# Kernel tuning notes

Hardware: AMD Instinct MI355X
Metric: run time of the kernel (lower is better)

## Reference

```python
import jax, jax.numpy as jnp
import numpy as np

T, IN, K, V = 4096, 512, 64, 64
H = K * V  # hidden_size = key_size * value_size
LN_EPS = 1e-5

def phi(x):
    return 1.0 + jax.nn.elu(x)

def mish(x):
    return x * jnp.tanh(jax.nn.softplus(x))

def setup_inputs() -> dict:
    key = jax.random.key(0)
    ks = jax.random.split(key, 12)
    def lin(k, out, inn):
        return (jax.random.normal(k, (out, inn), jnp.float32) / np.sqrt(inn).astype(np.float32))
    return {
        "x": jax.random.normal(ks[0], (T, IN), jnp.float32),
        "s0": jnp.zeros((1, K, V), jnp.float32),
        "z0": jnp.zeros((1, 1, K), jnp.float32),
        "start": jax.random.bernoulli(ks[1], 0.01, (T,)),
        "next_done": jax.random.bernoulli(ks[2], 0.01, (T,)),
        "Wk": lin(ks[3], K, IN), "Wq": lin(ks[4], K, IN),
        "Wv": lin(ks[5], V, IN), "bv": jnp.zeros((V,), jnp.float32),
        "Wskip": lin(ks[6], H, IN), "bskip": jnp.zeros((H,), jnp.float32),
        "W1": lin(ks[7], H, V), "b1": jnp.zeros((H,), jnp.float32),
        "W2": lin(ks[8], H, H), "b2": jnp.zeros((H,), jnp.float32),
        "W3": lin(ks[9], H, H), "b3": jnp.zeros((H,), jnp.float32),
        "ln_g": jnp.ones((H,), jnp.float32), "ln_b": jnp.zeros((H,), jnp.float32),
    }

def _combine(a, b):
    # associative update: later element's `start` resets accumulated (s, z)
    s1, z1, st1, d1 = a
    s2, z2, st2, d2 = b
    keep = jnp.logical_not(st2)
    return (s1 * keep + s2, z1 * keep + z2, jnp.logical_or(st2, st1), d2)

def reference(x, s0, z0, start, next_done, Wk, Wq, Wv, bv, Wskip, bskip,
              W1, b1, W2, b2, W3, b3, ln_g, ln_b):
    Tn = x.shape[0]
    k = phi(x @ Wk.T)           # [T, K]
    q = phi(x @ Wq.T)           # [T, K]
    v = x @ Wv.T + bv           # [T, V]
    kv = jnp.einsum('ti,tj->tij', k, v)  # [T, K, V]
    st = jnp.concatenate([jnp.zeros((1, 1, 1), bool), start.reshape(Tn, 1, 1)], 0)
    nd = jnp.concatenate([jnp.zeros((1, 1, 1), bool), next_done.reshape(Tn, 1, 1)], 0)
    kv = jnp.concatenate([s0, kv], 0)                        # [T+1, K, V]
    kk = jnp.concatenate([z0, k.reshape(Tn, 1, K)], 0)       # [T+1, 1, K]
    s, z, _, _ = jax.lax.associative_scan(_combine, (kv, kk, st, nd))
    s, z = s[1:], z[1:]
    numer = jnp.einsum('tij,ti->tj', s, q)                   # [T, V]
    # faithful to source: 'tzi,tj->tz' => sum_i z * sum_j q
    denom = jnp.einsum('tzi,tj->tz', z, q).clip(1e-6)        # [T, 1]
    out = numer / denom                                      # [T, V]
    h = mish(out @ W1.T + b1)
    h = mish(h @ W2.T + b2)
    h = h @ W3.T + b3
    h = h + (x @ Wskip.T + bskip)                            # mlp(out) + skip(x)
    mu = h.mean(-1, keepdims=True)
    var = ((h - mu) ** 2).mean(-1, keepdims=True)
    hn = (h - mu) / jnp.sqrt(var + LN_EPS) * ln_g + ln_b     # [T, H]
    return (hn, s, z)
```

## Files before the change

### kernel.cpp

```cpp
#include <hip/hip_runtime.h>
#include <math.h>

#define T_DIM 4096
#define IN_DIM 512
#define K_DIM 64
#define V_DIM 64
#define H_DIM 4096
#define CHUNKS 256
#define CLEN 16

typedef __attribute__((ext_vector_type(8))) short short8;
typedef __attribute__((ext_vector_type(4))) float f32x4;

__device__ __forceinline__ float phi_act(float v){
    return v > 0.f ? (v + 1.f) : (expm1f(v) + 1.f);
}
__device__ __forceinline__ float mish_act(float v){
    float sp = fmaxf(v, 0.f) + log1pf(expf(-fabsf(v)));
    return v * tanhf(sp);
}
__device__ __forceinline__ unsigned short f2bf(float f){
    union { float f; unsigned int u; } x; x.f = f;
    unsigned int u = x.u + 0x7fffu + ((x.u >> 16) & 1u);
    return (unsigned short)(u >> 16);
}

__device__ __forceinline__ void async16(const unsigned short* g, unsigned short* l){
    __builtin_amdgcn_global_load_lds(
        (const __attribute__((address_space(1))) unsigned int*)g,
        (__attribute__((address_space(3))) unsigned int*)l,
        16, 0, 0);
}

__device__ __forceinline__ short8 dsr128o(unsigned addr, int off){
    short8 d;
    asm volatile("ds_read_b128 %0, %1 offset:%2" : "=v"(d) : "v"(addr), "i"(off));
    return d;
}

#define LGKM(n)  asm volatile("s_waitcnt lgkmcnt(" #n ")" ::: "memory")
#define VMCNT(n) asm volatile("s_waitcnt vmcnt(" #n ")" ::: "memory")
#define SB0()    __builtin_amdgcn_sched_barrier(0)

#define CVT_X4   524288
#define CVT_WS   524288
#define CVT_W1   65536
#define CVT_W2   4194304
#define CVT_TOT  9502720
__global__ __launch_bounds__(256) void prep_kernel(
    const float* __restrict__ x,
    const float* __restrict__ Wk, const float* __restrict__ Wq, const float* __restrict__ Wv,
    const float* __restrict__ bv,
    float* __restrict__ kbuf, float* __restrict__ qbuf, float* __restrict__ vbuf,
    const float* __restrict__ Wskip, const float* __restrict__ W1,
    const float* __restrict__ W2, const float* __restrict__ W3,
    unsigned short* __restrict__ xb, unsigned short* __restrict__ Wskipb,
    unsigned short* __restrict__ W1b, unsigned short* __restrict__ W2b,
    unsigned short* __restrict__ W3b)
{
    __shared__ float As[16][68];
    __shared__ float Bs[16][68];
    const int bid = blockIdx.x;
    const int tid = threadIdx.x;

    if (bid < 192){
        const int which = bid >> 6;
        const float* B0 = which == 0 ? Wk : which == 1 ? Wq : Wv;
        float* Y        = which == 0 ? kbuf : which == 1 ? qbuf : vbuf;
        const int actp  = which < 2;
        const int bm    = (bid & 63) * 64;
        const int lrow  = tid >> 2;
        const int lk4   = (tid & 3) * 4;
        const int tm    = (tid >> 4) * 4;
        const int tn    = (tid & 15) * 4;
        float acc[4][4] = {};
        const float* aptr = x  + (size_t)(bm + lrow) * IN_DIM + lk4;
        const float* bptr = B0 + (size_t)lrow * IN_DIM + lk4;
        for (int k0 = 0; k0 < IN_DIM; k0 += 16){
            const float4 av  = *(const float4*)(aptr + k0);
            const float4 bv4 = *(const float4*)(bptr + k0);
            __syncthreads();
            As[lk4+0][lrow]=av.x;  As[lk4+1][lrow]=av.y;  As[lk4+2][lrow]=av.z;  As[lk4+3][lrow]=av.w;
            Bs[lk4+0][lrow]=bv4.x; Bs[lk4+1][lrow]=bv4.y; Bs[lk4+2][lrow]=bv4.z; Bs[lk4+3][lrow]=bv4.w;
            __syncthreads();
            #pragma unroll
            for (int kk = 0; kk < 16; ++kk){
                const float4 a = *(const float4*)&As[kk][tm];
                const float4 b = *(const float4*)&Bs[kk][tn];
                acc[0][0] += a.x*b.x; acc[0][1] += a.x*b.y; acc[0][2] += a.x*b.z; acc[0][3] += a.x*b.w;
                acc[1][0] += a.y*b.x; acc[1][1] += a.y*b.y; acc[1][2] += a.y*b.z; acc[1][3] += a.y*b.w;
                acc[2][0] += a.z*b.x; acc[2][1] += a.z*b.y; acc[2][2] += a.z*b.z; acc[2][3] += a.z*b.w;
                acc[3][0] += a.w*b.x; acc[3][1] += a.w*b.y; acc[3][2] += a.w*b.z; acc[3][3] += a.w*b.w;
            }
        }
        float badd[4] = {0.f, 0.f, 0.f, 0.f};
        if (which == 2){
            badd[0] = bv[tn+0]; badd[1] = bv[tn+1]; badd[2] = bv[tn+2]; badd[3] = bv[tn+3];
        }
        #pragma unroll
        for (int i = 0; i < 4; ++i){
            float r0 = acc[i][0] + badd[0];
            float r1 = acc[i][1] + badd[1];
            float r2 = acc[i][2] + badd[2];
            float r3 = acc[i][3] + badd[3];
            if (actp){ r0 = phi_act(r0); r1 = phi_act(r1); r2 = phi_act(r2); r3 = phi_act(r3); }
            *(float4*)&Y[(size_t)(bm + tm + i) * 64 + tn] = make_float4(r0, r1, r2, r3);
        }
        return;
    }

    const int nb = gridDim.x - 192;
    for (int i = (bid - 192) * 256 + tid; i < CVT_TOT; i += nb * 256){
        const float* src; unsigned short* dst; int off;
        if      (i < CVT_X4)                          { src = x;     dst = xb;     off = i; }
        else if (i < CVT_X4 + CVT_WS)                 { src = Wskip; dst = Wskipb; off = i - CVT_X4; }
        else if (i < CVT_X4 + CVT_WS + CVT_W1)        { src = W1;    dst = W1b;    off = i - CVT_X4 - CVT_WS; }
        else if (i < CVT_X4 + CVT_WS + CVT_W1 + CVT_W2){ src = W2;   dst = W2b;    off = i - CVT_X4 - CVT_WS - CVT_W1; }
        else                                          { src = W3;    dst = W3b;    off = i - CVT_X4 - CVT_WS - CVT_W1 - CVT_W2; }
        float4 v = ((const float4*)src)[off];
        ushort4 o;
        o.x = f2bf(v.x); o.y = f2bf(v.y); o.z = f2bf(v.z); o.w = f2bf(v.w);
        ((ushort4*)dst)[off] = o;
    }
}

__global__ __launch_bounds__(512, 2) void gemm256p(
    const unsigned short* __restrict__ A0, const unsigned short* __restrict__ B0, int K0,
    const unsigned short* __restrict__ A1, const unsigned short* __restrict__ B1, int K1,
    const float* __restrict__ bias0, const float* __restrict__ bias1,
    void* __restrict__ Y, int N, int act, int out_bf16)
{
    __shared__ unsigned short As[2][16384];
    __shared__ unsigned short Bs[2][16384];
    const int tid  = threadIdx.x;
    const int lane = tid & 63;
    const int w    = tid >> 6;
    const int wr   = w >> 2;
    const int wc   = w & 3;
    const int l15  = lane & 15;
    const int quad = lane >> 4;

    int bx = blockIdx.x, by = blockIdx.y;
    if (gridDim.x == 16 && gridDim.y == 16){
        const int id  = by * 16 + bx;
        const int xcd = id & 7;
        const int loc = id >> 3;
        bx = (xcd & 3) * 4 + (loc & 3);
        by = (xcd >> 2) * 8 + (loc >> 2);
    }
    const int bm = bx * 256;
    const int bn = by * 256;

    const int r0 = tid >> 3;
    const int kc = (tid & 7) ^ (r0 & 7);

    const unsigned asB = (unsigned)(size_t)&As[0][0];
    const unsigned bsB = (unsigned)(size_t)&Bs[0][0];
    const unsigned bA0 = asB + (unsigned)(((wr * 128 + l15) * 8 + ((0 + quad) ^ (l15 & 7))) * 16);
    const unsigned bA1 = asB + (unsigned)(((wr * 128 + l15) * 8 + ((4 + quad) ^ (l15 & 7))) * 16);
    const unsigned bB0 = bsB + (unsigned)(((wc * 64  + l15) * 8 + ((0 + quad) ^ (l15 & 7))) * 16);
    const unsigned bB1 = bsB + (unsigned)(((wc * 64  + l15) * 8 + ((4 + quad) ^ (l15 & 7))) * 16);

    f32x4 acc[8][4] = {};

    for (int seg = 0; seg < 2; ++seg){
        const unsigned short* A = seg ? A1 : A0;
        const unsigned short* B = seg ? B1 : B0;
        const int Kd = seg ? K1 : K0;
        if (Kd <= 0 || A == nullptr) continue;
        const int NT = Kd / 64;
        const size_t gstride = (size_t)64 * Kd;
        const unsigned short* pA = A + (size_t)bm * Kd + (size_t)r0 * Kd + kc * 8;
        const unsigned short* pB = B + (size_t)bn * Kd + (size_t)r0 * Kd + kc * 8;

        #pragma unroll
        for (int g = 0; g < 4; ++g) async16(pA + g * gstride, &As[0][(g * 512 + tid) * 8]);
        #pragma unroll
        for (int g = 0; g < 4; ++g) async16(pB + g * gstride, &Bs[0][(g * 512 + tid) * 8]);
        VMCNT(0);
        __builtin_amdgcn_s_barrier();

        for (int t = 0; t < NT; ++t){
            const unsigned bo = (unsigned)(t & 1) * 32768u;
            const unsigned aA0 = bA0 + bo, aA1 = bA1 + bo, aB0 = bB0 + bo, aB1 = bB1 + bo;
            short8 fa0[4], fa1[4], fb0[4], fb1[4];

            #pragma unroll
            for (int ni = 0; ni < 4; ++ni) fb0[ni] = dsr128o(aB0, ni * 2048);
            #pragma unroll
            for (int mi = 0; mi < 4; ++mi) fa0[mi] = dsr128o(aA0, mi * 2048);
            if (t + 1 < NT){
                const int bi = (t + 1) & 1;
                const int kn = (t + 1) * 64;
                #pragma unroll
                for (int g = 0; g < 4; ++g) async16(pA + g * gstride + kn, &As[bi][(g * 512 + tid) * 8]);
                #pragma unroll
                for (int g = 0; g < 4; ++g) async16(pB + g * gstride + kn, &Bs[bi][(g * 512 + tid) * 8]);
            }
            #pragma unroll
            for (int mi = 0; mi < 4; ++mi) fa1[mi] = dsr128o(aA0, (4 + mi) * 2048);

            __builtin_amdgcn_s_setprio(1);
            LGKM(7); SB0();
            #pragma unroll
            for (int ni = 0; ni < 4; ++ni)
                acc[0][ni] = __builtin_amdgcn_mfma_f32_16x16x32_bf16(fa0[0], fb0[ni], acc[0][ni], 0, 0, 0);
            LGKM(6); SB0();
            #pragma unroll
            for (int ni = 0; ni < 4; ++ni)
                acc[1][ni] = __builtin_amdgcn_mfma_f32_16x16x32_bf16(fa0[1], fb0[ni], acc[1][ni], 0, 0, 0);
            LGKM(5); SB0();
            #pragma unroll
            for (int ni = 0; ni < 4; ++ni)
                acc[2][ni] = __builtin_amdgcn_mfma_f32_16x16x32_bf16(fa0[2], fb0[ni], acc[2][ni], 0, 0, 0);
            LGKM(4); SB0();
            #pragma unroll
            for (int ni = 0; ni < 4; ++ni)
                acc[3][ni] = __builtin_amdgcn_mfma_f32_16x16x32_bf16(fa0[3], fb0[ni], acc[3][ni], 0, 0, 0);
            __builtin_amdgcn_s_setprio(0);

            #pragma unroll
            for (int ni = 0; ni < 4; ++ni) fb1[ni] = dsr128o(aB1, ni * 2048);
            #pragma unroll
            for (int mi = 0; mi < 4; ++mi) fa0[mi] = dsr128o(aA1, mi * 2048);

            __builtin_amdgcn_s_setprio(1);
            LGKM(11); SB0();
            #pragma unroll
            for (int ni = 0; ni < 4; ++ni)
                acc[4][ni] = __builtin_amdgcn_mfma_f32_16x16x32_bf16(fa1[0], fb0[ni], acc[4][ni], 0, 0, 0);
            LGKM(10); SB0();
            #pragma unroll
            for (int ni = 0; ni < 4; ++ni)
                acc[5][ni] = __builtin_amdgcn_mfma_f32_16x16x32_bf16(fa1[1], fb0[ni], acc[5][ni], 0, 0, 0);
            LGKM(9); SB0();
            #pragma unroll
            for (int ni = 0; ni < 4; ++ni)
                acc[6][ni] = __builtin_amdgcn_mfma_f32_16x16x32_bf16(fa1[2], fb0[ni], acc[6][ni], 0, 0, 0);
            LGKM(8); SB0();
            #pragma unroll
            for (int ni = 0; ni < 4; ++ni)
                acc[7][ni] = __builtin_amdgcn_mfma_f32_16x16x32_bf16(fa1[3], fb0[ni], acc[7][ni], 0, 0, 0);
            __builtin_amdgcn_s_setprio(0);

            #pragma unroll
            for (int mi = 0; mi < 4; ++mi) fa1[mi] = dsr128o(aA1, (4 + mi) * 2048);

            __builtin_amdgcn_s_setprio(1);
            LGKM(7); SB0();
            #pragma unroll
            for (int ni = 0; ni < 4; ++ni)
                acc[0][ni] = __builtin_amdgcn_mfma_f32_16x16x32_bf16(fa0[0], fb1[ni], acc[0][ni], 0, 0, 0);
            LGKM(6); SB0();
            #pragma unroll
            for (int ni = 0; ni < 4; ++ni)
                acc[1][ni] = __builtin_amdgcn_mfma_f32_16x16x32_bf16(fa0[1], fb1[ni], acc[1][ni], 0, 0, 0);
            LGKM(5); SB0();
            #pragma unroll
            for (int ni = 0; ni < 4; ++ni)
                acc[2][ni] = __builtin_amdgcn_mfma_f32_16x16x32_bf16(fa0[2], fb1[ni], acc[2][ni], 0, 0, 0);
            LGKM(4); SB0();
            #pragma unroll
            for (int ni = 0; ni < 4; ++ni)
                acc[3][ni] = __builtin_amdgcn_mfma_f32_16x16x32_bf16(fa0[3], fb1[ni], acc[3][ni], 0, 0, 0);

            LGKM(3); SB0();
            #pragma unroll
            for (int ni = 0; ni < 4; ++ni)
                acc[4][ni] = __builtin_amdgcn_mfma_f32_16x16x32_bf16(fa1[0], fb1[ni], acc[4][ni], 0, 0, 0);
            LGKM(2); SB0();
            #pragma unroll
            for (int ni = 0; ni < 4; ++ni)
                acc[5][ni] = __builtin_amdgcn_mfma_f32_16x16x32_bf16(fa1[1], fb1[ni], acc[5][ni], 0, 0, 0);
            LGKM(1); SB0();
            #pragma unroll
            for (int ni = 0; ni < 4; ++ni)
                acc[6][ni] = __builtin_amdgcn_mfma_f32_16x16x32_bf16(fa1[2], fb1[ni], acc[6][ni], 0, 0, 0);
            LGKM(0); SB0();
            #pragma unroll
            for (int ni = 0; ni < 4; ++ni)
                acc[7][ni] = __builtin_amdgcn_mfma_f32_16x16x32_bf16(fa1[3], fb1[ni], acc[7][ni], 0, 0, 0);
            __builtin_amdgcn_s_setprio(0);

            if (t + 1 < NT){
                VMCNT(0);
                __builtin_amdgcn_s_barrier();
            }
        }
    }

    #pragma unroll
    for (int ni = 0; ni < 4; ++ni){
        const int col = bn + wc * 64 + ni * 16 + l15;
        float bb = 0.f;
        if (bias0) bb += bias0[col];
        if (bias1) bb += bias1[col];
        #pragma unroll
        for (int mi = 0; mi < 8; ++mi){
            #pragma unroll
            for (int r = 0; r < 4; ++r){
                const int row = bm + wr * 128 + mi * 16 + quad * 4 + r;
                float v = acc[mi][ni][r] + bb;
                if (act == 2) v = mish_act(v);
                if (out_bf16) ((unsigned short*)Y)[(size_t)row * N + col] = f2bf(v);
                else          ((float*)Y)[(size_t)row * N + col] = v;
            }
        }
    }
}

__global__ __launch_bounds__(256) void scan_passA(
    const float* __restrict__ kbuf, const float* __restrict__ vbuf,
    const int* __restrict__ start,
    float* __restrict__ chunkS, float* __restrict__ chunkZ, int* __restrict__ chunkFlag)
{
    const int c   = blockIdx.x;
    const int tid = threadIdx.x;
    const int j   = tid >> 2;
    const int i0  = (tid & 3) * 16;
    __shared__ float k_lds[64], v_lds[64];
    float s_loc[16];
    #pragma unroll
    for (int e = 0; e < 16; ++e) s_loc[e] = 0.f;
    float z_loc = 0.f;
    int flag = 0;
    const int t0 = c * CLEN;
    for (int tt = 0; tt < CLEN; ++tt){
        const int t = t0 + tt;
        if (tid < 64)       k_lds[tid]      = kbuf[(size_t)t*K_DIM + tid];
        else if (tid < 128) v_lds[tid - 64] = vbuf[(size_t)t*V_DIM + tid - 64];
        __syncthreads();
        const int st = start[t];
        if (st){
            #pragma unroll
            for (int e = 0; e < 16; ++e) s_loc[e] = 0.f;
            z_loc = 0.f;
            flag = 1;
        }
        const float vj = v_lds[j];
        #pragma unroll
        for (int e = 0; e < 16; ++e) s_loc[e] += k_lds[i0 + e] * vj;
        if (tid < 64) z_loc += k_lds[tid];
        __syncthreads();
    }
    #pragma unroll
    for (int e = 0; e < 16; ++e) chunkS[(size_t)c*4096 + (i0 + e)*64 + j] = s_loc[e];
    if (tid < 64) chunkZ[c*64 + tid] = z_loc;
    if (tid == 0) chunkFlag[c] = flag;
}

__global__ __launch_bounds__(64) void scan_passB(
    const float* __restrict__ chunkS, const float* __restrict__ chunkZ, const int* __restrict__ chunkFlag,
    const float* __restrict__ s0, const float* __restrict__ z0,
    float* __restrict__ carryS, float* __restrict__ carryZ)
{
    const int ij = blockIdx.x * 64 + threadIdx.x;
    float e = s0[ij];
    for (int c = 0; c < CHUNKS; ++c){
        carryS[(size_t)c*4096 + ij] = e;
        const int f   = chunkFlag[c];
        const float s = chunkS[(size_t)c*4096 + ij];
        e = f ? s : (e + s);
    }
    if (ij < 64){
        float ez = z0[ij];
        for (int c = 0; c < CHUNKS; ++c){
            carryZ[c*64 + ij] = ez;
            const int f   = chunkFlag[c];
            const float z = chunkZ[c*64 + ij];
            ez = f ? z : (ez + z);
        }
    }
}

__global__ __launch_bounds__(256) void scan_passC(
    const float* __restrict__ kbuf, const float* __restrict__ vbuf, const float* __restrict__ qbuf,
    const int* __restrict__ start,
    const float* __restrict__ carryS, const float* __restrict__ carryZ,
    float* __restrict__ s_out, float* __restrict__ z_out, unsigned short* __restrict__ attout)
{
    const int c   = blockIdx.x;
    const int tid = threadIdx.x;
    const int j   = tid >> 2;
    const int g   = tid & 3;
    const int i0  = g * 16;
    __shared__ float k_lds[64], v_lds[64], q_lds[64];
    __shared__ float numer_lds[64];
    __shared__ float stage[4096];
    float s_loc[16];
    #pragma unroll
    for (int e = 0; e < 16; ++e) s_loc[e] = carryS[(size_t)c*4096 + (i0 + e)*64 + j];
    float z_loc = (tid < 64) ? carryZ[c*64 + tid] : 0.f;

    const int t0 = c * CLEN;
    for (int tt = 0; tt < CLEN; ++tt){
        const int t = t0 + tt;
        if (tid < 64)       k_lds[tid]       = kbuf[(size_t)t*K_DIM + tid];
        else if (tid < 128) v_lds[tid - 64]  = vbuf[(size_t)t*V_DIM + tid - 64];
        else if (tid < 192) q_lds[tid - 128] = qbuf[(size_t)t*K_DIM + tid - 128];
        __syncthreads();
        const int st = start[t];
        if (st){
            #pragma unroll
            for (int e = 0; e < 16; ++e) s_loc[e] = 0.f;
        }
        const float vj = v_lds[j];
        float np = 0.f;
        #pragma unroll
        for (int e = 0; e < 16; ++e){
            s_loc[e] += k_lds[i0 + e] * vj;
            np += s_loc[e] * q_lds[i0 + e];
        }
        np += __shfl_down(np, 1, 64);
        np += __shfl_down(np, 2, 64);
        if (g == 0) numer_lds[j] = np;
        float denom = 1.f;
        if (tid < 64){
            z_loc = (st ? 0.f : z_loc) + k_lds[tid];
            z_out[(size_t)t*K_DIM + tid] = z_loc;
            float zs = z_loc;
            float qs = q_lds[tid];
            #pragma unroll
            for (int o = 32; o > 0; o >>= 1){
                zs += __shfl_down(zs, o, 64);
                qs += __shfl_down(qs, o, 64);
            }
            zs = __shfl(zs, 0, 64);
            qs = __shfl(qs, 0, 64);
            denom = fmaxf(zs * qs, 1e-6f);
        }
        #pragma unroll
        for (int e = 0; e < 16; ++e) stage[(i0 + e)*64 + j] = s_loc[e];
        __syncthreads();
        float4* so = (float4*)(s_out + (size_t)t*4096);
        const float4* stv = (const float4*)stage;
        #pragma unroll
        for (int r = 0; r < 4; ++r) so[tid + 256*r] = stv[tid + 256*r];
        if (tid < 64) attout[(size_t)t*V_DIM + tid] = f2bf(numer_lds[tid] / denom);
        __syncthreads();
    }
}

__global__ __launch_bounds__(256) void ln_kernel(
    float* __restrict__ h, const float* __restrict__ g, const float* __restrict__ b)
{
    __shared__ float sm[4];
    const int t   = blockIdx.x;
    const int tid = threadIdx.x;
    float* row = h + (size_t)t * H_DIM;
    float4 v[4];
    float s = 0.f;
    #pragma unroll
    for (int r = 0; r < 4; ++r){
        v[r] = ((const float4*)row)[tid + 256*r];
        s += v[r].x + v[r].y + v[r].z + v[r].w;
    }
    #pragma unroll
    for (int o = 32; o > 0; o >>= 1) s += __shfl_down(s, o, 64);
    if ((tid & 63) == 0) sm[tid >> 6] = s;
    __syncthreads();
    const float mu = (sm[0] + sm[1] + sm[2] + sm[3]) * (1.f / H_DIM);
    __syncthreads();
    float sq = 0.f;
    #pragma unroll
    for (int r = 0; r < 4; ++r){
        float dx = v[r].x - mu, dy = v[r].y - mu, dz = v[r].z - mu, dw = v[r].w - mu;
        sq += dx*dx + dy*dy + dz*dz + dw*dw;
    }
    #pragma unroll
    for (int o = 32; o > 0; o >>= 1) sq += __shfl_down(sq, o, 64);
    if ((tid & 63) == 0) sm[tid >> 6] = sq;
    __syncthreads();
    const float var = (sm[0] + sm[1] + sm[2] + sm[3]) * (1.f / H_DIM);
    const float inv = rsqrtf(var + 1e-5f);
    #pragma unroll
    for (int r = 0; r < 4; ++r){
        const int i4 = tid + 256*r;
        const float4 gg = ((const float4*)g)[i4];
        const float4 bb = ((const float4*)b)[i4];
        float4 o;
        o.x = (v[r].x - mu) * inv * gg.x + bb.x;
        o.y = (v[r].y - mu) * inv * gg.y + bb.y;
        o.z = (v[r].z - mu) * inv * gg.z + bb.z;
        o.w = (v[r].w - mu) * inv * gg.w + bb.w;
        ((float4*)row)[i4] = o;
    }
}

extern "C" void kernel_launch(void* const* d_in, const int* in_sizes, int n_in,
                              void* d_out, int out_size, void* d_ws, size_t ws_size,
                              hipStream_t stream)
{
    (void)in_sizes; (void)n_in; (void)out_size; (void)ws_size;
    const float* x     = (const float*)d_in[0];
    const float* s0    = (const float*)d_in[1];
    const float* z0    = (const float*)d_in[2];
    const int*   start = (const int*)d_in[3];
    const float* Wk    = (const float*)d_in[5];
    const float* Wq    = (const float*)d_in[6];
    const float* Wv    = (const float*)d_in[7];
    const float* bv    = (const float*)d_in[8];
    const float* Wskip = (const float*)d_in[9];
    const float* bskip = (const float*)d_in[10];
    const float* W1    = (const float*)d_in[11];
    const float* b1    = (const float*)d_in[12];
    const float* W2    = (const float*)d_in[13];
    const float* b2    = (const float*)d_in[14];
    const float* W3    = (const float*)d_in[15];
    const float* b3    = (const float*)d_in[16];
    const float* ln_g  = (const float*)d_in[17];
    const float* ln_b  = (const float*)d_in[18];

    char* p = (char*)d_ws;
    auto alloc = [&](size_t bytes) -> void* {
        void* r = (void*)p; p += (bytes + 255) & ~(size_t)255; return r;
    };
    float* kbuf  = (float*)alloc((size_t)T_DIM * K_DIM * 4);
    float* qbuf  = (float*)alloc((size_t)T_DIM * K_DIM * 4);
    float* vbuf  = (float*)alloc((size_t)T_DIM * V_DIM * 4);
    float* chS   = (float*)alloc((size_t)CHUNKS * 4096 * 4);
    float* chZ   = (float*)alloc((size_t)CHUNKS * 64 * 4);
    float* caS   = (float*)alloc((size_t)CHUNKS * 4096 * 4);
    float* caZ   = (float*)alloc((size_t)CHUNKS * 64 * 4);
    int*   flags = (int*)  alloc((size_t)CHUNKS * 4);
    unsigned short* xb     = (unsigned short*)alloc((size_t)T_DIM * IN_DIM * 2);
    unsigned short* Wskipb = (unsigned short*)alloc((size_t)H_DIM * IN_DIM * 2);
    unsigned short* W1b    = (unsigned short*)alloc((size_t)H_DIM * V_DIM * 2);
    unsigned short* W2b    = (unsigned short*)alloc((size_t)H_DIM * H_DIM * 2);
    unsigned short* W3b    = (unsigned short*)alloc((size_t)H_DIM * H_DIM * 2);
    unsigned short* attb   = (unsigned short*)alloc((size_t)T_DIM * V_DIM * 2);
    unsigned short* h1b    = (unsigned short*)alloc((size_t)T_DIM * H_DIM * 2);
    unsigned short* h2b    = (unsigned short*)alloc((size_t)T_DIM * H_DIM * 2);

    float* hn  = (float*)d_out;
    float* s_o = hn  + (size_t)T_DIM * H_DIM;
    float* z_o = s_o + (size_t)T_DIM * K_DIM * V_DIM;

    prep_kernel<<<2048, 256, 0, stream>>>(x, Wk, Wq, Wv, bv, kbuf, qbuf, vbuf,
                                          Wskip, W1, W2, W3, xb, Wskipb, W1b, W2b, W3b);

    scan_passA<<<CHUNKS, 256, 0, stream>>>(kbuf, vbuf, start, chS, chZ, flags);
    scan_passB<<<64, 64, 0, stream>>>(chS, chZ, flags, s0, z0, caS, caZ);
    scan_passC<<<CHUNKS, 256, 0, stream>>>(kbuf, vbuf, qbuf, start, caS, caZ, s_o, z_o, attb);

    gemm256p<<<dim3(16, 16), 512, 0, stream>>>(
        attb, W1b, K_DIM, nullptr, nullptr, 0, b1, nullptr, h1b, H_DIM, 2, 1);
    gemm256p<<<dim3(16, 16), 512, 0, stream>>>(
        h1b, W2b, H_DIM, nullptr, nullptr, 0, b2, nullptr, h2b, H_DIM, 2, 1);
    gemm256p<<<dim3(16, 16), 512, 0, stream>>>(
        h2b, W3b, H_DIM, xb, Wskipb, IN_DIM, b3, bskip, hn, H_DIM, 0, 0);

    ln_kernel<<<T_DIM, 256, 0, stream>>>(hn, ln_g, ln_b);
}
```

Baseline: 758.6 us.

## Preload chunk k/v/q into LDS once and use cheaper exp-based mish

The scan passes now load all CLEN timesteps of k, v, q and the start flags into shared memory with one vectorized load at block start. This removes the per-timestep global loads and a barrier per step in pass A, and one barrier per step in pass C. Separately, mish is rewritten algebraically as v*(1-2/(e^v(e^v+2)+2)) using a single fast exp instead of log1p, exp and tanh. The new mish form can overflow to inf for large v, which still yields v*1, and is slightly less accurate.

```diff
diff --git a/kernel.cpp b/kernel.cpp
--- a/kernel.cpp
+++ b/kernel.cpp
@@ -16,8 +16,9 @@
     return v > 0.f ? (v + 1.f) : (expm1f(v) + 1.f);
 }
 __device__ __forceinline__ float mish_act(float v){
-    float sp = fmaxf(v, 0.f) + log1pf(expf(-fabsf(v)));
-    return v * tanhf(sp);
+    const float u = __expf(v);
+    const float w = u * (u + 2.f);
+    return v * (1.f - 2.f / (w + 2.f));
 }
 __device__ __forceinline__ unsigned short f2bf(float f){
     union { float f; unsigned int u; } x; x.f = f;
@@ -318,30 +319,29 @@
     const int tid = threadIdx.x;
     const int j   = tid >> 2;
     const int i0  = (tid & 3) * 16;
-    __shared__ float k_lds[64], v_lds[64];
+    __shared__ float k_lds[CLEN][64], v_lds[CLEN][64];
+    __shared__ int   st_lds[CLEN];
+    ((float4*)&k_lds[0][0])[tid] = ((const float4*)(kbuf + (size_t)c * CLEN * K_DIM))[tid];
+    ((float4*)&v_lds[0][0])[tid] = ((const float4*)(vbuf + (size_t)c * CLEN * V_DIM))[tid];
+    if (tid < CLEN) st_lds[tid] = start[c * CLEN + tid];
+    __syncthreads();
+
     float s_loc[16];
     #pragma unroll
     for (int e = 0; e < 16; ++e) s_loc[e] = 0.f;
     float z_loc = 0.f;
     int flag = 0;
-    const int t0 = c * CLEN;
     for (int tt = 0; tt < CLEN; ++tt){
-        const int t = t0 + tt;
-        if (tid < 64)       k_lds[tid]      = kbuf[(size_t)t*K_DIM + tid];
-        else if (tid < 128) v_lds[tid - 64] = vbuf[(size_t)t*V_DIM + tid - 64];
-        __syncthreads();
-        const int st = start[t];
-        if (st){
+        if (st_lds[tt]){
             #pragma unroll
             for (int e = 0; e < 16; ++e) s_loc[e] = 0.f;
             z_loc = 0.f;
             flag = 1;
         }
-        const float vj = v_lds[j];
-        #pragma unroll
-        for (int e = 0; e < 16; ++e) s_loc[e] += k_lds[i0 + e] * vj;
-        if (tid < 64) z_loc += k_lds[tid];
-        __syncthreads();
+        const float vj = v_lds[tt][j];
+        #pragma unroll
+        for (int e = 0; e < 16; ++e) s_loc[e] += k_lds[tt][i0 + e] * vj;
+        if (tid < 64) z_loc += k_lds[tt][tid];
     }
     #pragma unroll
     for (int e = 0; e < 16; ++e) chunkS[(size_t)c*4096 + (i0 + e)*64 + j] = s_loc[e];
@@ -384,42 +384,45 @@
     const int j   = tid >> 2;
     const int g   = tid & 3;
     const int i0  = g * 16;
-    __shared__ float k_lds[64], v_lds[64], q_lds[64];
+    __shared__ float k_lds[CLEN][64], v_lds[CLEN][64], q_lds[CLEN][64];
+    __shared__ int   st_lds[CLEN];
     __shared__ float numer_lds[64];
     __shared__ float stage[4096];
+    ((float4*)&k_lds[0][0])[tid] = ((const float4*)(kbuf + (size_t)c * CLEN * K_DIM))[tid];
+    ((float4*)&v_lds[0][0])[tid] = ((const float4*)(vbuf + (size_t)c * CLEN * V_DIM))[tid];
+    ((float4*)&q_lds[0][0])[tid] = ((const float4*)(qbuf + (size_t)c * CLEN * K_DIM))[tid];
+    if (tid < CLEN) st_lds[tid] = start[c * CLEN + tid];
+
     float s_loc[16];
     #pragma unroll
     for (int e = 0; e < 16; ++e) s_loc[e] = carryS[(size_t)c*4096 + (i0 + e)*64 + j];
     float z_loc = (tid < 64) ? carryZ[c*64 + tid] : 0.f;
+    __syncthreads();
 
     const int t0 = c * CLEN;
     for (int tt = 0; tt < CLEN; ++tt){
-        const int t = t0 + tt;
-        if (tid < 64)       k_lds[tid]       = kbuf[(size_t)t*K_DIM + tid];
-        else if (tid < 128) v_lds[tid - 64]  = vbuf[(size_t)t*V_DIM + tid - 64];
-        else if (tid < 192) q_lds[tid - 128] = qbuf[(size_t)t*K_DIM + tid - 128];
-        __syncthreads();
-        const int st = start[t];
+        const int t  = t0 + tt;
+        const int st = st_lds[tt];
         if (st){
             #pragma unroll
             for (int e = 0; e < 16; ++e) s_loc[e] = 0.f;
         }
-        const float vj = v_lds[j];
+        const float vj = v_lds[tt][j];
         float np = 0.f;
         #pragma unroll
         for (int e = 0; e < 16; ++e){
-            s_loc[e] += k_lds[i0 + e] * vj;
-            np += s_loc[e] * q_lds[i0 + e];
+            s_loc[e] += k_lds[tt][i0 + e] * vj;
+            np += s_loc[e] * q_lds[tt][i0 + e];
         }
         np += __shfl_down(np, 1, 64);
         np += __shfl_down(np, 2, 64);
         if (g == 0) numer_lds[j] = np;
         float denom = 1.f;
         if (tid < 64){
-            z_loc = (st ? 0.f : z_loc) + k_lds[tid];
+            z_loc = (st ? 0.f : z_loc) + k_lds[tt][tid];
             z_out[(size_t)t*K_DIM + tid] = z_loc;
             float zs = z_loc;
-            float qs = q_lds[tid];
+            float qs = q_lds[tt][tid];
             #pragma unroll
             for (int o = 32; o > 0; o >>= 1){
                 zs += __shfl_down(zs, o, 64);
```

Result: faster. 616.7 us (-18.7%).
